# Kernel optimization log

Hardware: AMD Instinct MI355X
Metric: run time of the kernel (lower is better)

The kernel has to match this reference:

```python
import jax, jax.numpy as jnp
import numpy as np

NEURONS = 54
DT = 4
STEPS = 30
POOL = 8

# SpikingNN: forward = (ex > 0).float(); backward = straight-through where ex > 0.
# Combined with nn.functional.threshold(rate, thr, 0), the spike output is
# (rate > thr).float() with gradient d spike/d rate = 1{rate > thr}.
@jax.custom_vjp
def spike(rate, thr):
    return (rate > thr).astype(rate.dtype)

def _spike_fwd(rate, thr):
    mask = rate > thr
    return mask.astype(rate.dtype), mask

def _spike_bwd(mask, g):
    return (g * mask.astype(g.dtype), jnp.zeros((), g.dtype))

spike.defvjp(_spike_fwd, _spike_bwd)

def setup_inputs() -> dict:
    key = jax.random.key(0)
    k1, k2, k3, k4, k5 = jax.random.split(key, 5)
    B = 16
    x = jax.random.normal(k1, (B, STEPS, 600, 600), jnp.float32)
    # small scales keep exp(current_sum) numerically stable
    fc_w = jax.random.normal(k2, (NEURONS, 75 * 75), jnp.float32) * 0.01
    fc_b = jax.random.normal(k3, (NEURONS,), jnp.float32) * 0.01
    l_weight = jax.random.uniform(k4, (NEURONS, DT), jnp.float32) * 0.01
    h_weight = jax.random.uniform(k5, (DT,), jnp.float32) * 0.01
    return {"x": x, "fc_w": fc_w, "fc_b": fc_b, "l_weight": l_weight, "h_weight": h_weight}

def reference(x, fc_w, fc_b, l_weight, h_weight):
    B = x.shape[0]
    H = x.shape[2] // POOL
    W = x.shape[3] // POOL
    # avg_pool2d(x, 8): non-overlapping 8x8 mean -> [B, 30, 75, 75]
    xp = x.reshape(B, STEPS, H, POOL, W, POOL).mean(axis=(3, 5))
    # per-frame fc: [B, 30, 5625] @ [5625, 54]^T + b -> [B, 30, 54]
    frames = jnp.einsum('btp,np->btn', xp.reshape(B, STEPS, H * W), fc_w) + fc_b
    count0 = jnp.zeros((B, NEURONS), x.dtype)
    hist0 = jnp.zeros((B, NEURONS, DT), x.dtype)

    def step(carry, frame):
        count, hist = carry                      # hist: [B, N, DT]
        hsum = hist * l_weight                   # [B, N, DT]
        lateral = hsum.sum(axis=(1, 2))[:, None] - hsum.sum(axis=2)  # [B, N]
        cur = frame + lateral + (hist * h_weight).sum(axis=2)
        rate = jnp.exp(cur)
        thr = jax.lax.stop_gradient(rate.mean())
        s = spike(rate, thr)                     # [B, N]
        hist = jnp.concatenate([hist[:, :, 1:], s[:, :, None]], axis=2)
        return (count + s, hist), None

    (count, _), _ = jax.lax.scan(step, (count0, hist0), jnp.swapaxes(frames, 0, 1))
    return jax.nn.softplus(count)
```

## Files before the change

### kernel.cpp

```cpp
#include <hip/hip_runtime.h>
#include <math.h>

#define NEURONS 54
#define DT 4
#define STEPS 30
#define BATCH 16
#define HW 75
#define P 5625
#define PPAD 5632
#define PPAD4 (PPAD/4)
#define NFRAMES (BATCH*STEPS)

__global__ void repack_w(const float* __restrict__ fc_w, float* __restrict__ wpad) {
    int idx = blockIdx.x * blockDim.x + threadIdx.x;
    if (idx >= NEURONS * PPAD) return;
    int n = idx / PPAD, p = idx % PPAD;
    wpad[idx] = (p < P) ? fc_w[n * P + p] : 0.0f;
}

__global__ __launch_bounds__(256) void pool_k(
    const float* __restrict__ x, float* __restrict__ xp) {
    int idx = blockIdx.x * 256 + threadIdx.x;
    int bt = idx / PPAD;
    int p  = idx - bt * PPAD;
    if (p >= P) { xp[idx] = 0.0f; return; }
    int ph = p / HW, pw = p - ph * HW;
    const float* base = x + (size_t)bt * (600 * 600) + (ph * 8) * 600 + pw * 8;
    float acc = 0.0f;
    #pragma unroll
    for (int r = 0; r < 8; r++) {
        const float4* row = (const float4*)(base + r * 600);
        float4 a = row[0], b4 = row[1];
        acc += (a.x + b4.x) + (a.y + b4.y) + (a.z + b4.z) + (a.w + b4.w);
    }
    xp[idx] = acc * (1.0f / 64.0f);
}

__global__ __launch_bounds__(512) void fc_k(
    const float* __restrict__ xp, const float* __restrict__ wpad,
    const float* __restrict__ fc_b, float* __restrict__ frames) {
    __shared__ __align__(16) float xp_s[PPAD];
    __shared__ float partial[NEURONS * 8];
    const int bt = blockIdx.x;
    const int tid = threadIdx.x;

    {
        const float4* src = (const float4*)(xp + bt * PPAD);
        float4* dst = (float4*)xp_s;
        for (int i = tid; i < PPAD4; i += 512) dst[i] = src[i];
    }
    __syncthreads();

    if (tid < NEURONS * 8) {
        int n = tid >> 3, c = tid & 7;
        const float4* w4 = (const float4*)(wpad + n * PPAD);
        const float4* x4 = (const float4*)xp_s;
        float acc = 0.0f;
        for (int i = c; i < PPAD4; i += 8) {
            float4 a = x4[i], w = w4[i];
            acc += a.x * w.x + a.y * w.y + a.z * w.z + a.w * w.w;
        }
        partial[tid] = acc;
    }
    __syncthreads();
    if (tid < NEURONS) {
        float s = 0.0f;
        #pragma unroll
        for (int c = 0; c < 8; c++) s += partial[tid * 8 + c];
        frames[bt * NEURONS + tid] = s + fc_b[tid];
    }
}

__global__ __launch_bounds__(1024) void scan_k(
    const float* __restrict__ frames, const float* __restrict__ l_weight,
    const float* __restrict__ h_weight, float* __restrict__ out) {
    __shared__ float fr_s[NFRAMES * NEURONS];
    __shared__ float wls[16];
    const int tid = threadIdx.x;
    const int b = tid >> 6;
    const int n = tid & 63;
    const bool active = (n < NEURONS);

    for (int i = tid; i < NFRAMES * NEURONS; i += 1024) fr_s[i] = frames[i];

    float lw[DT], hw_[DT];
    #pragma unroll
    for (int d = 0; d < DT; d++) {
        lw[d]  = active ? l_weight[n * DT + d] : 0.0f;
        hw_[d] = h_weight[d];
    }
    float hist[DT] = {0.f, 0.f, 0.f, 0.f};
    float count = 0.f;
    __syncthreads();

    for (int t = 0; t < STEPS; t++) {
        float my_hsum = 0.f, hterm = 0.f;
        #pragma unroll
        for (int d = 0; d < DT; d++) {
            my_hsum += hist[d] * lw[d];
            hterm   += hist[d] * hw_[d];
        }
        float tot = my_hsum;
        #pragma unroll
        for (int off = 32; off > 0; off >>= 1) tot += __shfl_xor(tot, off, 64);

        float rate = 0.f;
        if (active) {
            float cur = fr_s[(b * STEPS + t) * NEURONS + n] + (tot - my_hsum) + hterm;
            rate = expf(cur);
        }
        float rsum = rate;
        #pragma unroll
        for (int off = 32; off > 0; off >>= 1) rsum += __shfl_xor(rsum, off, 64);
        __syncthreads();
        if (n == 0) wls[b] = rsum;
        __syncthreads();
        float v = (n < 16) ? wls[n] : 0.f;
        #pragma unroll
        for (int off = 32; off > 0; off >>= 1) v += __shfl_xor(v, off, 64);
        float thr = v * (1.0f / (BATCH * NEURONS));

        float s = (active && rate > thr) ? 1.0f : 0.0f;
        count += s;
        hist[0] = hist[1]; hist[1] = hist[2]; hist[2] = hist[3]; hist[3] = s;
    }
    if (active) {
        out[b * NEURONS + n] = count + log1pf(expf(-count));
    }
}

extern "C" void kernel_launch(void* const* d_in, const int* in_sizes, int n_in,
                              void* d_out, int out_size, void* d_ws, size_t ws_size,
                              hipStream_t stream) {
    const float* x        = (const float*)d_in[0];
    const float* fc_w     = (const float*)d_in[1];
    const float* fc_b     = (const float*)d_in[2];
    const float* l_weight = (const float*)d_in[3];
    const float* h_weight = (const float*)d_in[4];
    float* out = (float*)d_out;

    float* wpad   = (float*)d_ws;
    float* xp     = wpad + NEURONS * PPAD;
    float* frames = xp + NFRAMES * PPAD;

    int wtotal = NEURONS * PPAD;
    repack_w<<<(wtotal + 511) / 512, 512, 0, stream>>>(fc_w, wpad);
    pool_k<<<(NFRAMES * PPAD) / 256, 256, 0, stream>>>(x, xp);
    fc_k<<<NFRAMES, 512, 0, stream>>>(xp, wpad, fc_b, frames);
    scan_k<<<1, 1024, 0, stream>>>(frames, l_weight, h_weight, out);
}
```

Before: 992.4 us.

## Fuse repack, pooling, fc and scan into one cooperative kernel

Replaces the four separate launches with a single cooperative kernel that uses grid-wide syncs between the weight repack/pooling stage, the per-frame fc stage, and the recurrent scan. Pooling threads now produce two adjacent pooled outputs each with wider row loads, and the scan packs two batches per wavefront in one 512-thread block. The aim is to remove launch overhead and inter-kernel gaps. In exchange, it limits the grid to 512 persistent blocks and adds grid-sync costs, with a fallback to the old path if the cooperative launch fails.

Result: slower. 1.374 ms (+38.4%).

```diff
diff --git a/kernel.cpp b/kernel.cpp
--- a/kernel.cpp
+++ b/kernel.cpp
@@ -1,5 +1,8 @@
 #include <hip/hip_runtime.h>
+#include <hip/hip_cooperative_groups.h>
 #include <math.h>
+
+namespace cg = cooperative_groups;
 
 #define NEURONS 54
 #define DT 4
@@ -10,6 +13,161 @@
 #define PPAD 5632
 #define PPAD4 (PPAD/4)
 #define NFRAMES (BATCH*STEPS)
+#define GRID 512
+#define TPB 512
+#define PAIRS (PPAD/2)
+
+__global__ __launch_bounds__(TPB, 4) void fused_all(
+    const float* __restrict__ x, const float* __restrict__ fc_w,
+    const float* __restrict__ fc_b, const float* __restrict__ l_weight,
+    const float* __restrict__ h_weight, float* __restrict__ wpad,
+    float* __restrict__ xp, float* __restrict__ frames,
+    float* __restrict__ out)
+{
+    __shared__ __align__(16) float xp_s[PPAD];
+    __shared__ float partial[NEURONS * 8];
+    __shared__ float wls[16];
+    cg::grid_group grid = cg::this_grid();
+    const int tid = threadIdx.x;
+    const int gid = blockIdx.x * TPB + tid;
+    const int gstride = GRID * TPB;
+
+    for (int idx = gid; idx < NEURONS * PPAD; idx += gstride) {
+        int n = idx / PPAD, p = idx - n * PPAD;
+        wpad[idx] = (p < P) ? fc_w[n * P + p] : 0.0f;
+    }
+
+    for (int g = gid; g < NFRAMES * PAIRS; g += gstride) {
+        int bt = g / PAIRS, tt = g - bt * PAIRS;
+        int p0 = tt * 2, p1 = p0 + 1;
+        const float* img = x + (size_t)bt * (600 * 600);
+        float v0 = 0.0f, v1 = 0.0f;
+        if (p0 < P) {
+            int ph = p0 / HW, pw = p0 - ph * HW;
+            const float* base = img + (ph * 8) * 600 + pw * 8;
+            float acc0 = 0.0f, acc1 = 0.0f;
+            if (pw < HW - 1) {
+                #pragma unroll
+                for (int r = 0; r < 8; r++) {
+                    const float4* row = (const float4*)(base + r * 600);
+                    float4 a = row[0], b4 = row[1], c = row[2], d4 = row[3];
+                    acc0 += (a.x + b4.x) + (a.y + b4.y) + (a.z + b4.z) + (a.w + b4.w);
+                    acc1 += (c.x + d4.x) + (c.y + d4.y) + (c.z + d4.z) + (c.w + d4.w);
+                }
+                v0 = acc0 * (1.0f / 64.0f);
+                v1 = acc1 * (1.0f / 64.0f);
+            } else {
+                #pragma unroll
+                for (int r = 0; r < 8; r++) {
+                    const float4* row = (const float4*)(base + r * 600);
+                    float4 a = row[0], b4 = row[1];
+                    acc0 += (a.x + b4.x) + (a.y + b4.y) + (a.z + b4.z) + (a.w + b4.w);
+                }
+                v0 = acc0 * (1.0f / 64.0f);
+                if (p1 < P) {
+                    int ph1 = p1 / HW, pw1 = p1 - ph1 * HW;
+                    const float* base1 = img + (ph1 * 8) * 600 + pw1 * 8;
+                    #pragma unroll
+                    for (int r = 0; r < 8; r++) {
+                        const float4* row = (const float4*)(base1 + r * 600);
+                        float4 a = row[0], b4 = row[1];
+                        acc1 += (a.x + b4.x) + (a.y + b4.y) + (a.z + b4.z) + (a.w + b4.w);
+                    }
+                    v1 = acc1 * (1.0f / 64.0f);
+                }
+            }
+        }
+        *(float2*)(xp + (size_t)bt * PPAD + p0) = make_float2(v0, v1);
+    }
+
+    __threadfence();
+    grid.sync();
+
+    if (blockIdx.x < NFRAMES) {
+        const int bt = blockIdx.x;
+        const float4* src = (const float4*)(xp + (size_t)bt * PPAD);
+        float4* dst = (float4*)xp_s;
+        for (int i = tid; i < PPAD4; i += TPB) dst[i] = src[i];
+        __syncthreads();
+        if (tid < NEURONS * 8) {
+            int n = tid >> 3, c = tid & 7;
+            const float4* w4 = (const float4*)(wpad + n * PPAD);
+            const float4* x4 = (const float4*)xp_s;
+            float acc = 0.0f;
+            for (int i = c; i < PPAD4; i += 8) {
+                float4 a = x4[i], w = w4[i];
+                acc += a.x * w.x + a.y * w.y + a.z * w.z + a.w * w.w;
+            }
+            partial[tid] = acc;
+        }
+        __syncthreads();
+        if (tid < NEURONS) {
+            float s = 0.0f;
+            #pragma unroll
+            for (int c = 0; c < 8; c++) s += partial[tid * 8 + c];
+            frames[bt * NEURONS + tid] = s + fc_b[tid];
+        }
+    }
+
+    __threadfence();
+    grid.sync();
+
+    if (blockIdx.x != 0) return;
+    const int w = tid >> 6, n = tid & 63;
+    const bool active = (n < NEURONS);
+    const int b0 = w, b1 = w + 8;
+    float lw[DT], hw_[DT];
+    #pragma unroll
+    for (int d = 0; d < DT; d++) {
+        lw[d]  = active ? l_weight[n * DT + d] : 0.0f;
+        hw_[d] = h_weight[d];
+    }
+    float hist0[DT] = {0.f,0.f,0.f,0.f}, hist1[DT] = {0.f,0.f,0.f,0.f};
+    float cnt0 = 0.f, cnt1 = 0.f;
+
+    for (int t = 0; t < STEPS; t++) {
+        float mh0 = 0.f, ht0 = 0.f, mh1 = 0.f, ht1 = 0.f;
+        #pragma unroll
+        for (int d = 0; d < DT; d++) {
+            mh0 += hist0[d] * lw[d];  ht0 += hist0[d] * hw_[d];
+            mh1 += hist1[d] * lw[d];  ht1 += hist1[d] * hw_[d];
+        }
+        float tot0 = mh0, tot1 = mh1;
+        #pragma unroll
+        for (int off = 32; off > 0; off >>= 1) {
+            tot0 += __shfl_xor(tot0, off, 64);
+            tot1 += __shfl_xor(tot1, off, 64);
+        }
+        float rate0 = 0.f, rate1 = 0.f;
+        if (active) {
+            rate0 = expf(frames[(b0 * STEPS + t) * NEURONS + n] + (tot0 - mh0) + ht0);
+            rate1 = expf(frames[(b1 * STEPS + t) * NEURONS + n] + (tot1 - mh1) + ht1);
+        }
+        float rs0 = rate0, rs1 = rate1;
+        #pragma unroll
+        for (int off = 32; off > 0; off >>= 1) {
+            rs0 += __shfl_xor(rs0, off, 64);
+            rs1 += __shfl_xor(rs1, off, 64);
+        }
+        __syncthreads();
+        if (n == 0) { wls[b0] = rs0; wls[b1] = rs1; }
+        __syncthreads();
+        float v = (n < 16) ? wls[n] : 0.f;
+        #pragma unroll
+        for (int off = 32; off > 0; off >>= 1) v += __shfl_xor(v, off, 64);
+        float thr = v * (1.0f / (BATCH * NEURONS));
+
+        float s0 = (active && rate0 > thr) ? 1.0f : 0.0f;
+        float s1 = (active && rate1 > thr) ? 1.0f : 0.0f;
+        cnt0 += s0; cnt1 += s1;
+        hist0[0]=hist0[1]; hist0[1]=hist0[2]; hist0[2]=hist0[3]; hist0[3]=s0;
+        hist1[0]=hist1[1]; hist1[1]=hist1[2]; hist1[2]=hist1[3]; hist1[3]=s1;
+    }
+    if (active) {
+        out[b0 * NEURONS + n] = cnt0 + log1pf(expf(-cnt0));
+        out[b1 * NEURONS + n] = cnt1 + log1pf(expf(-cnt1));
+    }
+}
 
 __global__ void repack_w(const float* __restrict__ fc_w, float* __restrict__ wpad) {
     int idx = blockIdx.x * blockDim.x + threadIdx.x;
@@ -43,14 +201,12 @@
     __shared__ float partial[NEURONS * 8];
     const int bt = blockIdx.x;
     const int tid = threadIdx.x;
-
     {
         const float4* src = (const float4*)(xp + bt * PPAD);
         float4* dst = (float4*)xp_s;
         for (int i = tid; i < PPAD4; i += 512) dst[i] = src[i];
     }
     __syncthreads();
-
     if (tid < NEURONS * 8) {
         int n = tid >> 3, c = tid & 7;
         const float4* w4 = (const float4*)(wpad + n * PPAD);
@@ -80,9 +236,7 @@
     const int b = tid >> 6;
     const int n = tid & 63;
     const bool active = (n < NEURONS);
-
     for (int i = tid; i < NFRAMES * NEURONS; i += 1024) fr_s[i] = frames[i];
-
     float lw[DT], hw_[DT];
     #pragma unroll
     for (int d = 0; d < DT; d++) {
@@ -92,7 +246,6 @@
     float hist[DT] = {0.f, 0.f, 0.f, 0.f};
     float count = 0.f;
     __syncthreads();
-
     for (int t = 0; t < STEPS; t++) {
         float my_hsum = 0.f, hterm = 0.f;
         #pragma unroll
@@ -103,7 +256,6 @@
         float tot = my_hsum;
         #pragma unroll
         for (int off = 32; off > 0; off >>= 1) tot += __shfl_xor(tot, off, 64);
-
         float rate = 0.f;
         if (active) {
             float cur = fr_s[(b * STEPS + t) * NEURONS + n] + (tot - my_hsum) + hterm;
@@ -119,7 +271,6 @@
         #pragma unroll
         for (int off = 32; off > 0; off >>= 1) v += __shfl_xor(v, off, 64);
         float thr = v * (1.0f / (BATCH * NEURONS));
-
         float s = (active && rate > thr) ? 1.0f : 0.0f;
         count += s;
         hist[0] = hist[1]; hist[1] = hist[2]; hist[2] = hist[3]; hist[3] = s;
@@ -143,9 +294,17 @@
     float* xp     = wpad + NEURONS * PPAD;
     float* frames = xp + NFRAMES * PPAD;
 
-    int wtotal = NEURONS * PPAD;
-    repack_w<<<(wtotal + 511) / 512, 512, 0, stream>>>(fc_w, wpad);
-    pool_k<<<(NFRAMES * PPAD) / 256, 256, 0, stream>>>(x, xp);
-    fc_k<<<NFRAMES, 512, 0, stream>>>(xp, wpad, fc_b, frames);
-    scan_k<<<1, 1024, 0, stream>>>(frames, l_weight, h_weight, out);
-}
+    void* args[] = { (void*)&x, (void*)&fc_w, (void*)&fc_b, (void*)&l_weight,
+                     (void*)&h_weight, (void*)&wpad, (void*)&xp, (void*)&frames,
+                     (void*)&out };
+    hipError_t err = hipLaunchCooperativeKernel((const void*)fused_all,
+                                                dim3(GRID), dim3(TPB),
+                                                args, 0, stream);
+    if (err != hipSuccess) {
+        int wtotal = NEURONS * PPAD;
+        repack_w<<<(wtotal + 511) / 512, 512, 0, stream>>>(fc_w, wpad);
+        pool_k<<<(NFRAMES * PPAD) / 256, 256, 0, stream>>>(x, xp);
+        fc_k<<<NFRAMES, 512, 0, stream>>>(xp, wpad, fc_b, frames);
+        scan_k<<<1, 1024, 0, stream>>>(frames, l_weight, h_weight, out);
+    }
+}
```
